# Performance work log

Hardware: AMD Instinct MI355X
Metric: run time of the kernel (lower is better)

## Reference

```python
import jax, jax.numpy as jnp
import numpy as np

EMBED_DIM = 1024
N_HEADS = 16
DK = EMBED_DIM // N_HEADS


def setup_inputs() -> dict:
    key = jax.random.key(0)
    ks = jax.random.split(key, 9)
    s = 1.0 / np.sqrt(EMBED_DIM)
    d = EMBED_DIM
    return {
        "x": jax.random.normal(ks[0], (2, 2048, d), dtype=jnp.float32),
        "Wq": jax.random.uniform(ks[1], (d, d), jnp.float32, -s, s),
        "bq": jax.random.uniform(ks[2], (d,), jnp.float32, -s, s),
        "Wk": jax.random.uniform(ks[3], (d, d), jnp.float32, -s, s),
        "bk": jax.random.uniform(ks[4], (d,), jnp.float32, -s, s),
        "Wv": jax.random.uniform(ks[5], (d, d), jnp.float32, -s, s),
        "bv": jax.random.uniform(ks[6], (d,), jnp.float32, -s, s),
        "Wo": jax.random.uniform(ks[7], (d, d), jnp.float32, -s, s),
        "bo": jax.random.uniform(ks[8], (d,), jnp.float32, -s, s),
    }


def reference(x, Wq, bq, Wk, bk, Wv, bv, Wo, bo):
    B, S, D = x.shape
    H, dk = N_HEADS, DK
    # QKV projections
    q = (x @ Wq + bq).reshape(B, S, H, dk).transpose(0, 2, 1, 3)  # [B,H,S,dk]
    k = (x @ Wk + bk).reshape(B, S, H, dk).transpose(0, 2, 1, 3)
    v = (x @ Wv + bv).reshape(B, S, H, dk).transpose(0, 2, 1, 3)
    # scaled dot-product attention with full score matrix (faithful to source)
    scores = jnp.einsum("bhqd,bhkd->bhqk", q, k) / jnp.sqrt(jnp.float32(dk))
    attn = jax.nn.softmax(scores, axis=-1)
    out = jnp.einsum("bhqk,bhkd->bhqd", attn, v)  # [B,H,S,dk]
    out = out.transpose(0, 2, 1, 3).reshape(B, S, D)
    return out @ Wo + bo
```

## Files before the change

### kernel.cpp

```cpp
#include <hip/hip_runtime.h>

typedef unsigned short u16;
typedef unsigned int u32;
typedef __attribute__((ext_vector_type(8))) short short8;
typedef __attribute__((ext_vector_type(4))) float float4v;

struct alignas(8) U16x4 { u16 x, y, z, w; };

__device__ __forceinline__ u16 f2b(float f) {
    union { float f; unsigned int u; } v; v.f = f;
    unsigned int r = (v.u >> 16) & 1u;
    v.u += 0x7fffu + r;
    return (u16)(v.u >> 16);
}

__device__ __forceinline__ float b2f(u16 u) {
    union { unsigned int u; float f; } v; v.u = ((u32)u) << 16; return v.f;
}

__device__ __forceinline__ void gld16(const u16* g, u16* l) {
    __builtin_amdgcn_global_load_lds(
        (const __attribute__((address_space(1))) void*)g,
        (__attribute__((address_space(3))) void*)l, 16, 0, 0);
}

__device__ __forceinline__ short8 frag8(const u16* base, int row, int cg) {
    return *(const short8*)(base + row * 64 + ((cg ^ (row & 7)) << 3));
}

__global__ __launch_bounds__(256) void prep_kernel(
    const float* __restrict__ x, const float* __restrict__ W0,
    const float* __restrict__ W1, const float* __restrict__ W2,
    const float* __restrict__ W3, u16* __restrict__ xb,
    u16* __restrict__ T0, u16* __restrict__ T1,
    u16* __restrict__ T2, u16* __restrict__ T3) {
    __shared__ float tile[32][33];
    int id = blockIdx.x;
    if (id < 4096) {
        size_t i = ((size_t)id * 256 + threadIdx.x) * 4;
        float4 v = *(const float4*)(x + i);
        U16x4 o;
        o.x = f2b(v.x); o.y = f2b(v.y); o.z = f2b(v.z); o.w = f2b(v.w);
        *(U16x4*)(xb + i) = o;
        return;
    }
    int r = id - 4096;
    int z = r >> 10, tl = r & 1023;
    const float* W = (z == 0) ? W0 : (z == 1) ? W1 : (z == 2) ? W2 : W3;
    u16* T = (z == 0) ? T0 : (z == 1) ? T1 : (z == 2) ? T2 : T3;
    int t = threadIdx.x;
    int tx = t & 31, ty = t >> 5;
    int bn = (tl & 31) * 32, bk = (tl >> 5) * 32;
#pragma unroll
    for (int p = 0; p < 4; ++p) {
        int k = ty + p * 8;
        tile[k][tx] = W[(size_t)(bk + k) * 1024 + bn + tx];
    }
    __syncthreads();
#pragma unroll
    for (int p = 0; p < 4; ++p) {
        int n = ty + p * 8;
        T[(size_t)(bn + n) * 1024 + bk + tx] = f2b(tile[tx][n]);
    }
}

__device__ __forceinline__ void gemm_core_gld(const u16* __restrict__ A,
                                              const u16* __restrict__ BT,
                                              int m0, int n0, int t,
                                              u16* As, u16* Bs,
                                              float4v acc[4][4]) {
    int lane = t & 63, wid = t >> 6;
    int wr = wid >> 1, wc = wid & 1;
    int l16 = lane & 15, quad = lane >> 4;
    int rl = lane >> 3, cs = lane & 7;

    for (int k0 = 0; k0 < 1024; k0 += 64) {
        __syncthreads();
#pragma unroll
        for (int p = 0; p < 4; ++p) {
            int blk = wid * 4 + p;
            int row = blk * 8 + rl;
            int c = cs ^ (row & 7);
            gld16(A + (size_t)(m0 + row) * 1024 + k0 + c * 8, As + blk * 512);
            gld16(BT + (size_t)(n0 + row) * 1024 + k0 + c * 8, Bs + blk * 512);
        }
        __syncthreads();
#pragma unroll
        for (int ks = 0; ks < 64; ks += 32) {
            int cg = (ks >> 3) + quad;
            short8 af[4], bf[4];
#pragma unroll
            for (int i = 0; i < 4; ++i) af[i] = frag8(As, wr * 64 + i * 16 + l16, cg);
#pragma unroll
            for (int j = 0; j < 4; ++j) bf[j] = frag8(Bs, wc * 64 + j * 16 + l16, cg);
#pragma unroll
            for (int i = 0; i < 4; ++i)
#pragma unroll
                for (int j = 0; j < 4; ++j)
                    acc[i][j] = __builtin_amdgcn_mfma_f32_16x16x32_bf16(
                        af[i], bf[j], acc[i][j], 0, 0, 0);
        }
    }
}

__global__ __launch_bounds__(256) void qkv_kernel(
    const u16* __restrict__ X,
    const u16* __restrict__ WqT, const u16* __restrict__ WkT, const u16* __restrict__ WvT,
    const float* __restrict__ bq, const float* __restrict__ bk, const float* __restrict__ bv,
    u16* __restrict__ Qo, u16* __restrict__ Ko, u16* __restrict__ VTo) {
    __shared__ __align__(16) u16 As[128 * 64];
    __shared__ __align__(16) u16 Bs[128 * 64];
    int id = blockIdx.x;
    int m = (id & 7) | (((id >> 3) & 3) << 3);
    int nz = id >> 5;
    int n = nz & 7, z = nz >> 3;
    const u16* BT = (z == 0) ? WqT : (z == 1) ? WkT : WvT;
    const float* bias = (z == 0) ? bq : (z == 1) ? bk : bv;
    int t = threadIdx.x;
    int m0 = m * 128, n0 = n * 128;

    float4v acc[4][4];
    float4v zero4 = {0.f, 0.f, 0.f, 0.f};
#pragma unroll
    for (int i = 0; i < 4; ++i)
#pragma unroll
        for (int j = 0; j < 4; ++j) acc[i][j] = zero4;

    gemm_core_gld(X, BT, m0, n0, t, As, Bs, acc);

    int lane = t & 63, wid = t >> 6;
    int wr = wid >> 1, wc = wid & 1;
    int l16 = lane & 15, quad = lane >> 4;
    float scale = (z == 0) ? 0.18033688011112042f : 1.0f;

#pragma unroll
    for (int j = 0; j < 4; ++j) {
        int n1 = n0 + wc * 64 + j * 16 + l16;
        float bvl = bias[n1];
#pragma unroll
        for (int i = 0; i < 4; ++i) {
            int mbase = m0 + wr * 64 + i * 16 + quad * 4;
            if (z < 2) {
                u16* out = (z == 0) ? Qo : Ko;
#pragma unroll
                for (int r = 0; r < 4; ++r)
                    out[(size_t)(mbase + r) * 1024 + n1] =
                        f2b((acc[i][j][r] + bvl) * scale);
            } else {
                int bidx = mbase >> 11, s = mbase & 2047;
                size_t base =
                    ((size_t)((bidx * 16 + (n1 >> 6)) * 64 + (n1 & 63))) * 2048 + s;
                U16x4 pk;
                pk.x = f2b(acc[i][j][0] + bvl);
                pk.y = f2b(acc[i][j][1] + bvl);
                pk.z = f2b(acc[i][j][2] + bvl);
                pk.w = f2b(acc[i][j][3] + bvl);
                *(U16x4*)(VTo + base) = pk;
            }
        }
    }
}

__global__ __launch_bounds__(512) void oproj_kernel(const u16* __restrict__ X,
                                                    const u16* __restrict__ WoT,
                                                    const float* __restrict__ bias,
                                                    float* __restrict__ out) {
    __shared__ __align__(16) u16 As[128 * 64];
    __shared__ __align__(16) u16 Bs[128 * 64];
    int id = blockIdx.x;
    int m = (id & 7) | (((id >> 3) & 3) << 3);
    int n = id >> 5;
    int t = threadIdx.x;
    int m0 = m * 128, n0 = n * 128;
    int lane = t & 63, wid = t >> 6;
    int wr = wid >> 2, wc = wid & 3;
    int l16 = lane & 15, quad = lane >> 4;
    int rl = lane >> 3, cs = lane & 7;

    float4v acc[4][2];
    float4v zero4 = {0.f, 0.f, 0.f, 0.f};
#pragma unroll
    for (int i = 0; i < 4; ++i)
#pragma unroll
        for (int j = 0; j < 2; ++j) acc[i][j] = zero4;

    for (int k0 = 0; k0 < 1024; k0 += 64) {
        __syncthreads();
#pragma unroll
        for (int p = 0; p < 2; ++p) {
            int blk = wid * 2 + p;
            int row = blk * 8 + rl;
            int c = cs ^ (row & 7);
            gld16(X + (size_t)(m0 + row) * 1024 + k0 + c * 8, As + blk * 512);
            gld16(WoT + (size_t)(n0 + row) * 1024 + k0 + c * 8, Bs + blk * 512);
        }
        __syncthreads();
#pragma unroll
        for (int ks = 0; ks < 64; ks += 32) {
            int cg = (ks >> 3) + quad;
            short8 af[4], bf[2];
#pragma unroll
            for (int i = 0; i < 4; ++i) af[i] = frag8(As, wr * 64 + i * 16 + l16, cg);
#pragma unroll
            for (int j = 0; j < 2; ++j) bf[j] = frag8(Bs, wc * 32 + j * 16 + l16, cg);
#pragma unroll
            for (int i = 0; i < 4; ++i)
#pragma unroll
                for (int j = 0; j < 2; ++j)
                    acc[i][j] = __builtin_amdgcn_mfma_f32_16x16x32_bf16(
                        af[i], bf[j], acc[i][j], 0, 0, 0);
        }
    }

#pragma unroll
    for (int j = 0; j < 2; ++j) {
        int n1 = n0 + wc * 32 + j * 16 + l16;
        float bvl = bias[n1];
#pragma unroll
        for (int i = 0; i < 4; ++i) {
            int mbase = m0 + wr * 64 + i * 16 + quad * 4;
#pragma unroll
            for (int r = 0; r < 4; ++r)
                out[(size_t)(mbase + r) * 1024 + n1] = acc[i][j][r] + bvl;
        }
    }
}

__global__ __launch_bounds__(128, 2) void flash_kernel(const u16* __restrict__ Q,
                                                       const u16* __restrict__ Kn,
                                                       const u16* __restrict__ VT,
                                                       u16* __restrict__ Opart,
                                                       float* __restrict__ lpart) {
    __shared__ __align__(16) u16 Ks[64 * 64];
    __shared__ __align__(16) u16 Vs[64 * 64];
    __shared__ __align__(16) u16 Ps[128][72];

    int id = blockIdx.x;
    int bh = (id & 7) | (((id >> 3) & 3) << 3);
    int rest = id >> 5;
    int qb = rest & 15, kvz = rest >> 4;
    int b = bh >> 4, h = bh & 15;
    int t = threadIdx.x;
    int wid = t >> 6, lane = t & 63;
    int l16 = lane & 15, quad = lane >> 4;
    int rl = lane >> 3, cs = lane & 7;
    int q0 = qb * 128 + wid * 64;
    size_t kbase = (size_t)(b * 2048) * 1024 + h * 64;
    size_t vbase = (size_t)(bh * 64) * 2048;

    short8 qf[4][2];
#pragma unroll
    for (int j = 0; j < 4; ++j)
#pragma unroll
        for (int kk = 0; kk < 2; ++kk)
            qf[j][kk] = *(const short8*)(
                Q + ((size_t)(b * 2048 + q0 + j * 16 + l16)) * 1024 + h * 64 +
                kk * 32 + quad * 8);

    float4v oacc[4][4], lacc[4];
    float4v zero4 = {0.f, 0.f, 0.f, 0.f};
#pragma unroll
    for (int ip = 0; ip < 4; ++ip) {
        lacc[ip] = zero4;
#pragma unroll
        for (int jd = 0; jd < 4; ++jd) oacc[ip][jd] = zero4;
    }

    const short ONE = (short)0x3F80;
    short8 ones = {ONE, ONE, ONE, ONE, ONE, ONE, ONE, ONE};

    for (int kvi = 0; kvi < 16; ++kvi) {
        int kv = kvz * 1024 + kvi * 64;
        __syncthreads();
        if (wid == 0) {
#pragma unroll
            for (int p = 0; p < 8; ++p) {
                int row = p * 8 + rl;
                int c = cs ^ (row & 7);
                gld16(Kn + kbase + (size_t)(kv + row) * 1024 + c * 8, Ks + p * 512);
            }
        } else {
#pragma unroll
            for (int p = 0; p < 8; ++p) {
                int row = p * 8 + rl;
                int c = cs ^ (row & 7);
                gld16(VT + vbase + (size_t)row * 2048 + kv + c * 8, Vs + p * 512);
            }
        }
        __syncthreads();

#pragma unroll
        for (int i = 0; i < 4; ++i) {
            float4v sacc[4];
#pragma unroll
            for (int j = 0; j < 4; ++j) sacc[j] = zero4;
#pragma unroll
            for (int kk = 0; kk < 2; ++kk) {
                short8 kf = frag8(Ks, i * 16 + l16, kk * 4 + quad);
#pragma unroll
                for (int j = 0; j < 4; ++j)
                    sacc[j] = __builtin_amdgcn_mfma_f32_16x16x32_bf16(
                        kf, qf[j][kk], sacc[j], 0, 0, 0);
            }
#pragma unroll
            for (int j = 0; j < 4; ++j) {
                u32 e0 = __float_as_uint(__builtin_amdgcn_exp2f(sacc[j][0])) + 0x8000u;
                u32 e1 = __float_as_uint(__builtin_amdgcn_exp2f(sacc[j][1])) + 0x8000u;
                u32 e2 = __float_as_uint(__builtin_amdgcn_exp2f(sacc[j][2])) + 0x8000u;
                u32 e3 = __float_as_uint(__builtin_amdgcn_exp2f(sacc[j][3])) + 0x8000u;
                uint2 pk;
                pk.x = __builtin_amdgcn_perm(e1, e0, 0x07060302u);
                pk.y = __builtin_amdgcn_perm(e3, e2, 0x07060302u);
                *(uint2*)(&Ps[wid * 64 + j * 16 + l16][i * 16 + quad * 4]) = pk;
            }
        }

#pragma unroll
        for (int kk = 0; kk < 2; ++kk) {
            int cg = kk * 4 + quad;
            short8 pf[4];
#pragma unroll
            for (int ip = 0; ip < 4; ++ip)
                pf[ip] = *(const short8*)(
                    &Ps[wid * 64 + ip * 16 + l16][kk * 32 + quad * 8]);
#pragma unroll
            for (int jd = 0; jd < 4; ++jd) {
                short8 vf = frag8(Vs, jd * 16 + l16, cg);
#pragma unroll
                for (int ip = 0; ip < 4; ++ip)
                    oacc[ip][jd] = __builtin_amdgcn_mfma_f32_16x16x32_bf16(
                        pf[ip], vf, oacc[ip][jd], 0, 0, 0);
            }
#pragma unroll
            for (int ip = 0; ip < 4; ++ip)
                lacc[ip] = __builtin_amdgcn_mfma_f32_16x16x32_bf16(
                    pf[ip], ones, lacc[ip], 0, 0, 0);
        }
    }

    size_t obase = (size_t)kvz * 4194304;
#pragma unroll
    for (int ip = 0; ip < 4; ++ip)
#pragma unroll
        for (int r = 0; r < 4; ++r) {
            int q = q0 + ip * 16 + quad * 4 + r;
#pragma unroll
            for (int jd = 0; jd < 4; ++jd)
                Opart[obase + ((size_t)(b * 2048 + q)) * 1024 + h * 64 +
                      jd * 16 + l16] = f2b(oacc[ip][jd][r]);
        }
    if (l16 == 0) {
#pragma unroll
        for (int ip = 0; ip < 4; ++ip)
#pragma unroll
            for (int r = 0; r < 4; ++r) {
                int q = q0 + ip * 16 + quad * 4 + r;
                lpart[kvz * 65536 + (b * 2048 + q) * 16 + h] = lacc[ip][r];
            }
    }
}

__global__ __launch_bounds__(256) void combine_kernel(const u16* __restrict__ Op,
                                                      const float* __restrict__ lp,
                                                      u16* __restrict__ out) {
    int idx = blockIdx.x * 256 + threadIdx.x;
    size_t i = (size_t)idx * 4;
    int qg = idx >> 8;
    int d = (idx & 255) * 4;
    int h = d >> 6;
    float l0 = lp[qg * 16 + h], l1 = lp[65536 + qg * 16 + h];
    float inv = 1.0f / (l0 + l1);
    U16x4 o0 = *(const U16x4*)(Op + i);
    U16x4 o1 = *(const U16x4*)(Op + 4194304 + i);
    U16x4 o;
    o.x = f2b((b2f(o0.x) + b2f(o1.x)) * inv);
    o.y = f2b((b2f(o0.y) + b2f(o1.y)) * inv);
    o.z = f2b((b2f(o0.z) + b2f(o1.z)) * inv);
    o.w = f2b((b2f(o0.w) + b2f(o1.w)) * inv);
    *(U16x4*)(out + i) = o;
}

extern "C" void kernel_launch(void* const* d_in, const int* in_sizes, int n_in,
                              void* d_out, int out_size, void* d_ws, size_t ws_size,
                              hipStream_t stream) {
    const float* x  = (const float*)d_in[0];
    const float* Wq = (const float*)d_in[1];
    const float* bq = (const float*)d_in[2];
    const float* Wk = (const float*)d_in[3];
    const float* bk = (const float*)d_in[4];
    const float* Wv = (const float*)d_in[5];
    const float* bv = (const float*)d_in[6];
    const float* Wo = (const float*)d_in[7];
    const float* bo = (const float*)d_in[8];
    float* out = (float*)d_out;

    char* ws = (char*)d_ws;
    const size_t MB = 1024 * 1024;
    u16* xb  = (u16*)(ws);
    u16* wqt = (u16*)(ws + 8 * MB);
    u16* wkt = (u16*)(ws + 10 * MB);
    u16* wvt = (u16*)(ws + 12 * MB);
    u16* wot = (u16*)(ws + 14 * MB);
    u16* qb_ = (u16*)(ws + 16 * MB);
    u16* kb_ = (u16*)(ws + 24 * MB);
    u16* vt_ = (u16*)(ws + 32 * MB);
    u16* ab_ = (u16*)(ws + 40 * MB);
    u16* op_ = (u16*)(ws + 48 * MB);
    float* lp_ = (float*)(ws + 64 * MB);

    prep_kernel<<<8192, 256, 0, stream>>>(x, Wq, Wk, Wv, Wo, xb,
                                          wqt, wkt, wvt, wot);
    qkv_kernel<<<768, 256, 0, stream>>>(xb, wqt, wkt, wvt, bq, bk, bv,
                                        qb_, kb_, vt_);
    flash_kernel<<<1024, 128, 0, stream>>>(qb_, kb_, vt_, op_, lp_);
    combine_kernel<<<4096, 256, 0, stream>>>(op_, lp_, ab_);
    oproj_kernel<<<256, 512, 0, stream>>>(ab_, wot, bo, out);
}
```

Baseline: 202.9 us.

## Fuse split-KV combine into output projection A-tile load

Removes the separate combine kernel and has the output-projection GEMM read both partial attention outputs and their softmax denominators directly, normalising and packing to bf16 before writing the swizzled A tile into LDS. This drops one launch and the round trip of the combined activation through global memory. In exchange, the A-operand load switches from asynchronous global-to-LDS copies to synchronous register loads plus per-element arithmetic. Each partial is also re-read by every N-tile of the projection, so total global reads increase. A dead duplicate assignment to s0 is left in the code.

```diff
diff --git a/kernel.cpp b/kernel.cpp
--- a/kernel.cpp
+++ b/kernel.cpp
@@ -14,8 +14,11 @@
     return (u16)(v.u >> 16);
 }
 
-__device__ __forceinline__ float b2f(u16 u) {
-    union { unsigned int u; float f; } v; v.u = ((u32)u) << 16; return v.f;
+__device__ __forceinline__ float b2f_lo(u32 u) {
+    union { unsigned int u; float f; } v; v.u = u << 16; return v.f;
+}
+__device__ __forceinline__ float b2f_hi(u32 u) {
+    union { unsigned int u; float f; } v; v.u = u & 0xffff0000u; return v.f;
 }
 
 __device__ __forceinline__ void gld16(const u16* g, u16* l) {
@@ -161,7 +164,8 @@
     }
 }
 
-__global__ __launch_bounds__(512) void oproj_kernel(const u16* __restrict__ X,
+__global__ __launch_bounds__(512) void oproj_kernel(const u16* __restrict__ Op,
+                                                    const float* __restrict__ lp,
                                                     const u16* __restrict__ WoT,
                                                     const float* __restrict__ bias,
                                                     float* __restrict__ out) {
@@ -185,14 +189,34 @@
         for (int j = 0; j < 2; ++j) acc[i][j] = zero4;
 
     for (int k0 = 0; k0 < 1024; k0 += 64) {
+        int head = k0 >> 6;
         __syncthreads();
 #pragma unroll
         for (int p = 0; p < 2; ++p) {
             int blk = wid * 2 + p;
             int row = blk * 8 + rl;
             int c = cs ^ (row & 7);
-            gld16(X + (size_t)(m0 + row) * 1024 + k0 + c * 8, As + blk * 512);
             gld16(WoT + (size_t)(n0 + row) * 1024 + k0 + c * 8, Bs + blk * 512);
+            size_t off = (size_t)(m0 + row) * 1024 + k0 + c * 8;
+            uint4 a0 = *(const uint4*)(Op + off);
+            uint4 a1 = *(const uint4*)(Op + 4194304 + off);
+            float l0 = lp[(m0 + row) * 16 + head];
+            float l1 = lp[65536 + (m0 + row) * 16 + head];
+            float inv = 1.0f / (l0 + l1);
+            uint4 pk;
+            u32 s0, s1;
+            s0 = f2b(b2f_lo(a0.x) + b2f_lo(a1.x)) | ((u32)f2b((b2f_hi(a0.x) + b2f_hi(a1.x)) * inv) << 16);
+            s0 = (u32)f2b((b2f_lo(a0.x) + b2f_lo(a1.x)) * inv) |
+                 ((u32)f2b((b2f_hi(a0.x) + b2f_hi(a1.x)) * inv) << 16);
+            s1 = (u32)f2b((b2f_lo(a0.y) + b2f_lo(a1.y)) * inv) |
+                 ((u32)f2b((b2f_hi(a0.y) + b2f_hi(a1.y)) * inv) << 16);
+            pk.x = s0; pk.y = s1;
+            s0 = (u32)f2b((b2f_lo(a0.z) + b2f_lo(a1.z)) * inv) |
+                 ((u32)f2b((b2f_hi(a0.z) + b2f_hi(a1.z)) * inv) << 16);
+            s1 = (u32)f2b((b2f_lo(a0.w) + b2f_lo(a1.w)) * inv) |
+                 ((u32)f2b((b2f_hi(a0.w) + b2f_hi(a1.w)) * inv) << 16);
+            pk.z = s0; pk.w = s1;
+            *(uint4*)(As + blk * 512 + lane * 8) = pk;
         }
         __syncthreads();
 #pragma unroll
@@ -358,26 +382,6 @@
                 lpart[kvz * 65536 + (b * 2048 + q) * 16 + h] = lacc[ip][r];
             }
     }
-}
-
-__global__ __launch_bounds__(256) void combine_kernel(const u16* __restrict__ Op,
-                                                      const float* __restrict__ lp,
-                                                      u16* __restrict__ out) {
-    int idx = blockIdx.x * 256 + threadIdx.x;
-    size_t i = (size_t)idx * 4;
-    int qg = idx >> 8;
-    int d = (idx & 255) * 4;
-    int h = d >> 6;
-    float l0 = lp[qg * 16 + h], l1 = lp[65536 + qg * 16 + h];
-    float inv = 1.0f / (l0 + l1);
-    U16x4 o0 = *(const U16x4*)(Op + i);
-    U16x4 o1 = *(const U16x4*)(Op + 4194304 + i);
-    U16x4 o;
-    o.x = f2b((b2f(o0.x) + b2f(o1.x)) * inv);
-    o.y = f2b((b2f(o0.y) + b2f(o1.y)) * inv);
-    o.z = f2b((b2f(o0.z) + b2f(o1.z)) * inv);
-    o.w = f2b((b2f(o0.w) + b2f(o1.w)) * inv);
-    *(U16x4*)(out + i) = o;
 }
 
 extern "C" void kernel_launch(void* const* d_in, const int* in_sizes, int n_in,
@@ -404,15 +408,13 @@
     u16* qb_ = (u16*)(ws + 16 * MB);
     u16* kb_ = (u16*)(ws + 24 * MB);
     u16* vt_ = (u16*)(ws + 32 * MB);
-    u16* ab_ = (u16*)(ws + 40 * MB);
-    u16* op_ = (u16*)(ws + 48 * MB);
-    float* lp_ = (float*)(ws + 64 * MB);
+    u16* op_ = (u16*)(ws + 40 * MB);
+    float* lp_ = (float*)(ws + 56 * MB);
 
     prep_kernel<<<8192, 256, 0, stream>>>(x, Wq, Wk, Wv, Wo, xb,
                                           wqt, wkt, wvt, wot);
     qkv_kernel<<<768, 256, 0, stream>>>(xb, wqt, wkt, wvt, bq, bk, bv,
                                         qb_, kb_, vt_);
     flash_kernel<<<1024, 128, 0, stream>>>(qb_, kb_, vt_, op_, lp_);
-    combine_kernel<<<4096, 256, 0, stream>>>(op_, lp_, ab_);
-    oproj_kernel<<<256, 512, 0, stream>>>(ab_, wot, bo, out);
-}
+    oproj_kernel<<<256, 512, 0, stream>>>(op_, lp_, wot, bo, out);
+}
```

Measured after the change: 207.6 us. 1.02x slower.

## Fuse Q, K, V projections into one block sharing the X tile

Applied to the files above, without the earlier changes.

The QKV GEMM now computes all three projections in a single 512-thread block. Each block loads one X tile and three weight tiles per k-step, so X is reused across Q, K and V instead of being loaded three times by separate blocks. The grid shrinks from 768 to 256 blocks, and LDS grows to four 128x64 tiles. This trades fewer redundant global loads for lower block count and higher register pressure (24 accumulators per wave), which may reduce occupancy on a 256-CU device.

```diff
diff --git a/kernel.cpp b/kernel.cpp
--- a/kernel.cpp
+++ b/kernel.cpp
@@ -64,99 +64,96 @@
     }
 }
 
-__device__ __forceinline__ void gemm_core_gld(const u16* __restrict__ A,
-                                              const u16* __restrict__ BT,
-                                              int m0, int n0, int t,
-                                              u16* As, u16* Bs,
-                                              float4v acc[4][4]) {
-    int lane = t & 63, wid = t >> 6;
-    int wr = wid >> 1, wc = wid & 1;
-    int l16 = lane & 15, quad = lane >> 4;
-    int rl = lane >> 3, cs = lane & 7;
-
-    for (int k0 = 0; k0 < 1024; k0 += 64) {
-        __syncthreads();
-#pragma unroll
-        for (int p = 0; p < 4; ++p) {
-            int blk = wid * 4 + p;
-            int row = blk * 8 + rl;
-            int c = cs ^ (row & 7);
-            gld16(A + (size_t)(m0 + row) * 1024 + k0 + c * 8, As + blk * 512);
-            gld16(BT + (size_t)(n0 + row) * 1024 + k0 + c * 8, Bs + blk * 512);
-        }
-        __syncthreads();
-#pragma unroll
-        for (int ks = 0; ks < 64; ks += 32) {
-            int cg = (ks >> 3) + quad;
-            short8 af[4], bf[4];
-#pragma unroll
-            for (int i = 0; i < 4; ++i) af[i] = frag8(As, wr * 64 + i * 16 + l16, cg);
-#pragma unroll
-            for (int j = 0; j < 4; ++j) bf[j] = frag8(Bs, wc * 64 + j * 16 + l16, cg);
-#pragma unroll
-            for (int i = 0; i < 4; ++i)
-#pragma unroll
-                for (int j = 0; j < 4; ++j)
-                    acc[i][j] = __builtin_amdgcn_mfma_f32_16x16x32_bf16(
-                        af[i], bf[j], acc[i][j], 0, 0, 0);
-        }
-    }
-}
-
-__global__ __launch_bounds__(256) void qkv_kernel(
+
+__global__ __launch_bounds__(512, 2) void qkv_kernel(
     const u16* __restrict__ X,
     const u16* __restrict__ WqT, const u16* __restrict__ WkT, const u16* __restrict__ WvT,
     const float* __restrict__ bq, const float* __restrict__ bk, const float* __restrict__ bv,
     u16* __restrict__ Qo, u16* __restrict__ Ko, u16* __restrict__ VTo) {
     __shared__ __align__(16) u16 As[128 * 64];
-    __shared__ __align__(16) u16 Bs[128 * 64];
+    __shared__ __align__(16) u16 Bs[3][128 * 64];
     int id = blockIdx.x;
     int m = (id & 7) | (((id >> 3) & 3) << 3);
-    int nz = id >> 5;
-    int n = nz & 7, z = nz >> 3;
-    const u16* BT = (z == 0) ? WqT : (z == 1) ? WkT : WvT;
-    const float* bias = (z == 0) ? bq : (z == 1) ? bk : bv;
+    int n = id >> 5;
     int t = threadIdx.x;
     int m0 = m * 128, n0 = n * 128;
-
-    float4v acc[4][4];
+    int lane = t & 63, wid = t >> 6;
+    int wr = wid >> 2, wc = wid & 3;
+    int l16 = lane & 15, quad = lane >> 4;
+    int rl = lane >> 3, cs = lane & 7;
+
+    int tileid = wid >> 1, half = wid & 1;
+    const u16* gsrc = (tileid == 0) ? X : (tileid == 1) ? WqT
+                     : (tileid == 2) ? WkT : WvT;
+    int gbase = (tileid == 0) ? m0 : n0;
+    u16* ldst = (tileid == 0) ? As : &Bs[tileid - 1][0];
+
+    float4v acc[3][4][2];
     float4v zero4 = {0.f, 0.f, 0.f, 0.f};
 #pragma unroll
-    for (int i = 0; i < 4; ++i)
-#pragma unroll
-        for (int j = 0; j < 4; ++j) acc[i][j] = zero4;
-
-    gemm_core_gld(X, BT, m0, n0, t, As, Bs, acc);
-
-    int lane = t & 63, wid = t >> 6;
-    int wr = wid >> 1, wc = wid & 1;
-    int l16 = lane & 15, quad = lane >> 4;
-    float scale = (z == 0) ? 0.18033688011112042f : 1.0f;
-
-#pragma unroll
-    for (int j = 0; j < 4; ++j) {
-        int n1 = n0 + wc * 64 + j * 16 + l16;
-        float bvl = bias[n1];
+    for (int z = 0; z < 3; ++z)
+#pragma unroll
+        for (int i = 0; i < 4; ++i)
+#pragma unroll
+            for (int j = 0; j < 2; ++j) acc[z][i][j] = zero4;
+
+    for (int k0 = 0; k0 < 1024; k0 += 64) {
+        __syncthreads();
+#pragma unroll
+        for (int p = 0; p < 8; ++p) {
+            int q = half * 8 + p;
+            int row = q * 8 + rl;
+            int c = cs ^ (row & 7);
+            gld16(gsrc + (size_t)(gbase + row) * 1024 + k0 + c * 8, ldst + q * 512);
+        }
+        __syncthreads();
+#pragma unroll
+        for (int ks = 0; ks < 64; ks += 32) {
+            int cg = (ks >> 3) + quad;
+            short8 af[4];
+#pragma unroll
+            for (int i = 0; i < 4; ++i)
+                af[i] = frag8(As, wr * 64 + i * 16 + l16, cg);
+#pragma unroll
+            for (int z = 0; z < 3; ++z) {
+                short8 bf[2];
+#pragma unroll
+                for (int j = 0; j < 2; ++j)
+                    bf[j] = frag8(&Bs[z][0], wc * 32 + j * 16 + l16, cg);
+#pragma unroll
+                for (int i = 0; i < 4; ++i)
+#pragma unroll
+                    for (int j = 0; j < 2; ++j)
+                        acc[z][i][j] = __builtin_amdgcn_mfma_f32_16x16x32_bf16(
+                            af[i], bf[j], acc[z][i][j], 0, 0, 0);
+            }
+        }
+    }
+
+    const float QSCALE = 0.18033688011112042f;
+#pragma unroll
+    for (int j = 0; j < 2; ++j) {
+        int n1 = n0 + wc * 32 + j * 16 + l16;
+        float bql = bq[n1], bkl = bk[n1], bvl = bv[n1];
 #pragma unroll
         for (int i = 0; i < 4; ++i) {
             int mbase = m0 + wr * 64 + i * 16 + quad * 4;
-            if (z < 2) {
-                u16* out = (z == 0) ? Qo : Ko;
-#pragma unroll
-                for (int r = 0; r < 4; ++r)
-                    out[(size_t)(mbase + r) * 1024 + n1] =
-                        f2b((acc[i][j][r] + bvl) * scale);
-            } else {
-                int bidx = mbase >> 11, s = mbase & 2047;
-                size_t base =
-                    ((size_t)((bidx * 16 + (n1 >> 6)) * 64 + (n1 & 63))) * 2048 + s;
-                U16x4 pk;
-                pk.x = f2b(acc[i][j][0] + bvl);
-                pk.y = f2b(acc[i][j][1] + bvl);
-                pk.z = f2b(acc[i][j][2] + bvl);
-                pk.w = f2b(acc[i][j][3] + bvl);
-                *(U16x4*)(VTo + base) = pk;
-            }
+#pragma unroll
+            for (int r = 0; r < 4; ++r) {
+                Qo[(size_t)(mbase + r) * 1024 + n1] =
+                    f2b((acc[0][i][j][r] + bql) * QSCALE);
+                Ko[(size_t)(mbase + r) * 1024 + n1] =
+                    f2b(acc[1][i][j][r] + bkl);
+            }
+            int bidx = mbase >> 11, s = mbase & 2047;
+            size_t base =
+                ((size_t)((bidx * 16 + (n1 >> 6)) * 64 + (n1 & 63))) * 2048 + s;
+            U16x4 pk;
+            pk.x = f2b(acc[2][i][j][0] + bvl);
+            pk.y = f2b(acc[2][i][j][1] + bvl);
+            pk.z = f2b(acc[2][i][j][2] + bvl);
+            pk.w = f2b(acc[2][i][j][3] + bvl);
+            *(U16x4*)(VTo + base) = pk;
         }
     }
 }
@@ -410,7 +407,7 @@
 
     prep_kernel<<<8192, 256, 0, stream>>>(x, Wq, Wk, Wv, Wo, xb,
                                           wqt, wkt, wvt, wot);
-    qkv_kernel<<<768, 256, 0, stream>>>(xb, wqt, wkt, wvt, bq, bk, bv,
+    qkv_kernel<<<256, 512, 0, stream>>>(xb, wqt, wkt, wvt, bq, bk, bv,
                                         qb_, kb_, vt_);
     flash_kernel<<<1024, 128, 0, stream>>>(qb_, kb_, vt_, op_, lp_);
     combine_kernel<<<4096, 256, 0, stream>>>(op_, lp_, ab_);
```

Result: faster. 192.9 us (-5.0%).
